# Performance work log

Measured on AMD Instinct MI355X. Metric: run time of the kernel, lower is better.

The kernel has to match this reference:

```python
import jax, jax.numpy as jnp
import numpy as np

GRID_SIZE = 5
SPLINE_ORDER = 3
N_COEFF = GRID_SIZE + SPLINE_ORDER  # 8 basis functions per input feature
D_MODEL = 1024
D_FF = 4096


def make_grid(in_features):
    # uniform grid on [-1, 1] extended by spline_order knots each side
    h = 2.0 / GRID_SIZE
    g = np.arange(-SPLINE_ORDER, GRID_SIZE + SPLINE_ORDER + 1, dtype=np.float32) * h - 1.0
    return jnp.asarray(np.tile(g[None, :], (in_features, 1)))  # (in, G + 2k + 1)


def b_splines(x, grid):
    # x: (N, in) -> (N, in, G + k) via Cox-de Boor recursion
    xe = x[..., None]
    bases = ((xe >= grid[:, :-1]) & (xe < grid[:, 1:])).astype(x.dtype)
    for j in range(1, SPLINE_ORDER + 1):
        left = (xe - grid[:, : -(j + 1)]) / (grid[:, j:-1] - grid[:, : -(j + 1)])
        right = (grid[:, j + 1 :] - xe) / (grid[:, j + 1 :] - grid[:, 1:-j])
        bases = left * bases[..., :-1] + right * bases[..., 1:]
    return bases


def kan_linear(x, base_w, spline_w, grid):
    # x: (N, in); base_w: (out, in); spline_w: (out, in, C)
    base = jax.nn.silu(x) @ base_w.T
    b = b_splines(x, grid)                      # (N, in, C)
    spl = jnp.einsum('nic,oic->no', b, spline_w)
    return base + spl


def setup_inputs() -> dict:
    key = jax.random.key(0)
    ks = jax.random.split(key, 7)
    s_in = 1.0 / np.sqrt(D_MODEL)
    s_ff = 1.0 / np.sqrt(D_FF)
    return {
        'x': jax.random.normal(ks[0], (2, 2048, D_MODEL), jnp.float32),
        'base_w1': jax.random.normal(ks[1], (D_FF, D_MODEL), jnp.float32) * s_in,
        'spline_w1': jax.random.normal(ks[2], (D_FF, D_MODEL, N_COEFF), jnp.float32) * s_in * 0.1,
        'base_w2': jax.random.normal(ks[3], (D_FF, D_MODEL), jnp.float32) * s_in,
        'spline_w2': jax.random.normal(ks[4], (D_FF, D_MODEL, N_COEFF), jnp.float32) * s_in * 0.1,
        'base_w3': jax.random.normal(ks[5], (D_MODEL, D_FF), jnp.float32) * s_ff,
        'spline_w3': jax.random.normal(ks[6], (D_MODEL, D_FF, N_COEFF), jnp.float32) * s_ff * 0.1,
        'grid_in': make_grid(D_MODEL),
        'grid_ff': make_grid(D_FF),
    }


def reference(x, base_w1, spline_w1, base_w2, spline_w2, base_w3, spline_w3, grid_in, grid_ff):
    shp = x.shape
    x2 = x.reshape(-1, shp[-1])                      # (N, d_model)
    h = kan_linear(x2, base_w1, spline_w1, grid_in) * kan_linear(x2, base_w2, spline_w2, grid_in)
    out = kan_linear(h, base_w3, spline_w3, grid_ff)
    return out.reshape(shp)
```

## Files before the change

### kernel.cpp

```cpp
#include <hip/hip_runtime.h>
#include <hip/hip_bf16.h>
#include <cstdint>
#include <cstddef>
#include <type_traits>


#define D_MODEL 1024
#define D_FF    4096
#define NTOK    4096
#define NC      9
#define K1      (D_MODEL * NC)
#define K3      (D_FF * NC)
#define SPLITK2 16
#define SPLITKF 4
#define CHUNK   1024
#define SLOT    65536

typedef __attribute__((ext_vector_type(8))) short bf16x8;
typedef __attribute__((ext_vector_type(4))) float f32x4;

__device__ __forceinline__ unsigned short bf16b(float f) {
  __hip_bfloat16 h = __float2bfloat16(f);
  return __builtin_bit_cast(unsigned short, h);
}
__device__ __forceinline__ uint32_t pk2(float a, float b) {
  return (uint32_t)bf16b(a) | ((uint32_t)bf16b(b) << 16);
}

__device__ __forceinline__ void kan_feat_u(float x, unsigned short* dst) {
  float s = x / (1.0f + __expf(-x));
  float B[11];
#pragma unroll
  for (int j = 0; j < 11; ++j) {
    float gj = -2.2f + 0.4f * j;
    B[j] = (x >= gj && x < gj + 0.4f) ? 1.0f : 0.0f;
  }
#pragma unroll
  for (int p = 1; p <= 3; ++p) {
    float inv = 1.0f / (0.4f * p);
#pragma unroll
    for (int i = 0; i + p < 11; ++i) {
      float gi = -2.2f + 0.4f * i;
      B[i] = (x - gi) * inv * B[i] + ((gi + 0.4f + 0.4f * p) - x) * inv * B[i + 1];
    }
  }
  dst[0] = bf16b(s);
#pragma unroll
  for (int c = 0; c < 8; ++c) dst[1 + c] = bf16b(B[c]);
}

__global__ void pack_kan_w(const float* __restrict__ bw, const float* __restrict__ sw,
                           __hip_bfloat16* __restrict__ W, int K, int inShift,
                           int rowMul, int rowBase, size_t totalPairs) {
  size_t t = (size_t)blockIdx.x * blockDim.x + threadIdx.x;
  if (t >= totalPairs) return;
  const int halfShift = inShift - 1;
  size_t o = t >> halfShift;
  size_t p = t & (((size_t)1 << halfShift) - 1);
  size_t e0 = (o << inShift) + 2 * p;
  float2 b = *(const float2*)(bw + e0);
  const float4* sp = (const float4*)(sw + e0 * 8);
  float4 s0 = sp[0], s1 = sp[1], s2 = sp[2], s3 = sp[3];
  const size_t HP = (size_t)1 << halfShift;
  uint32_t* dst = (uint32_t*)(W + (o * rowMul + rowBase) * (size_t)K);
  dst[p]          = pk2(b.x, b.y);
  dst[1 * HP + p] = pk2(s0.x, s2.x);
  dst[2 * HP + p] = pk2(s0.y, s2.y);
  dst[3 * HP + p] = pk2(s0.z, s2.z);
  dst[4 * HP + p] = pk2(s0.w, s2.w);
  dst[5 * HP + p] = pk2(s1.x, s3.x);
  dst[6 * HP + p] = pk2(s1.y, s3.y);
  dst[7 * HP + p] = pk2(s1.z, s3.z);
  dst[8 * HP + p] = pk2(s1.w, s3.w);
}

__global__ void build_a1(const float* __restrict__ x, __hip_bfloat16* __restrict__ A1) {
  size_t t = (size_t)blockIdx.x * blockDim.x + threadIdx.x;
  if (t >= (size_t)NTOK * D_MODEL / 2) return;
  size_t n = t >> 9;
  size_t p = t & 511;
  float2 xv = *(const float2*)(x + n * D_MODEL + 2 * p);
  unsigned short h0[9], h1[9];
  kan_feat_u(xv.x, h0);
  kan_feat_u(xv.y, h1);
  uint32_t* dst = (uint32_t*)(A1 + n * (size_t)K1);
#pragma unroll
  for (int f = 0; f < 9; ++f)
    dst[(size_t)f * 512 + p] = (uint32_t)h0[f] | ((uint32_t)h1[f] << 16);
}

template <typename HT>
__global__ void glu_a3(const HT* __restrict__ Hc, __hip_bfloat16* __restrict__ A3c) {
  size_t t = (size_t)blockIdx.x * blockDim.x + threadIdx.x;
  if (t >= (size_t)CHUNK * D_FF / 2) return;
  size_t n = t >> 11;
  size_t p = t & 2047;
  float a0, a1, c0, c1;
  if constexpr (std::is_same<HT, float>::value) {
    float2 u = *(const float2*)(Hc + n * 8192 + 2 * p);
    float2 v = *(const float2*)(Hc + n * 8192 + 4096 + 2 * p);
    a0 = u.x; a1 = u.y; c0 = v.x; c1 = v.y;
  } else {
    a0 = __bfloat162float(Hc[n * 8192 + 2 * p]);
    a1 = __bfloat162float(Hc[n * 8192 + 2 * p + 1]);
    c0 = __bfloat162float(Hc[n * 8192 + 4096 + 2 * p]);
    c1 = __bfloat162float(Hc[n * 8192 + 4096 + 2 * p + 1]);
  }
  unsigned short h0[9], h1[9];
  kan_feat_u(a0 * c0, h0);
  kan_feat_u(a1 * c1, h1);
  uint32_t* dst = (uint32_t*)(A3c + n * (size_t)K3);
#pragma unroll
  for (int f = 0; f < 9; ++f)
    dst[(size_t)f * 2048 + p] = (uint32_t)h0[f] | ((uint32_t)h1[f] << 16);
}

#define STAGE(Ts)                                                                        \
  {                                                                                      \
    const int _sl = ((Ts) & 1) * SLOT;                                                   \
    const size_t _ko = (size_t)(Ts) * 128;                                               \
    _Pragma("unroll") for (int _st = 0; _st < 4; ++_st) {                                \
      __builtin_amdgcn_global_load_lds(                                                  \
          (const __attribute__((address_space(1))) void*)(gA0 + _st * strideK + _ko),    \
          (__attribute__((address_space(3))) void*)(lds_raw + _sl + _st * 8192 + dW),    \
          16, 0, 0);                                                                     \
      __builtin_amdgcn_global_load_lds(                                                  \
          (const __attribute__((address_space(1))) void*)(gB0 + _st * strideK + _ko),    \
          (__attribute__((address_space(3))) void*)(lds_raw + _sl + 32768 +              \
                                                    _st * 8192 + dW),                    \
          16, 0, 0);                                                                     \
    }                                                                                    \
  }

template <typename CT, bool FUSE>
__global__ __launch_bounds__(512, 2) void gemm256(
    const __hip_bfloat16* __restrict__ A, const __hip_bfloat16* __restrict__ Bw,
    CT* __restrict__ Cp, int N, int K, int kLen,
    __hip_bfloat16* __restrict__ A3out) {
  __shared__ __align__(16) char lds_raw[2 * SLOT];

  const int tid = threadIdx.x;
  const int wid = tid >> 6, lane = tid & 63;
  const int wr = wid >> 2, wc = wid & 3;

  const int nwg = gridDim.x * gridDim.y;
  const int orig = blockIdx.y * gridDim.x + blockIdx.x;
  const int q = nwg >> 3, r = nwg & 7;
  const int xcd = orig & 7, lid = orig >> 3;
  const int wg = (xcd < r ? xcd * (q + 1) : r * (q + 1) + (xcd - r) * q) + lid;
  const int bx = wg % gridDim.x, by = wg / gridDim.x;

  const size_t brow = (size_t)by * 256;
  const size_t bcol = (size_t)bx * 256;
  const int kStart = (int)blockIdx.z * kLen;
  const int NT = kLen / 64;

  const int kbx = (lane & 7) ^ (lane >> 3);
  const int rsub = lane >> 3;
  const size_t strideK = (size_t)K * 128;
  const char* gA0 = (const char*)A +
      ((brow + (size_t)(wid * 8 + rsub)) * (size_t)K + kStart + kbx * 8) * 2;
  const char* gB0 = (const char*)Bw +
      ((bcol + (size_t)(wid * 8 + rsub)) * (size_t)K + kStart + kbx * 8) * 2;
  const int dW = wid * 1024;

  const int gx0 = (((lane >> 4) ^ (lane & 7))) * 16;
  const int gx1 = ((((lane >> 4) + 4) ^ (lane & 7))) * 16;
  const int arow = (wr * 128 + (lane & 15)) * 128;
  const int brw = 32768 + (wc * 64 + (lane & 15)) * 128;

  f32x4 acc[8][4] = {};

  STAGE(0);
  asm volatile("s_waitcnt vmcnt(0)" ::: "memory");
  __builtin_amdgcn_s_barrier();

  for (int T = 0; T < NT; ++T) {
    if (T + 1 < NT) STAGE(T + 1);

    const int sl = (T & 1) * SLOT;
    bf16x8 af[8], bfr[4];
#pragma unroll
    for (int mf = 0; mf < 8; ++mf)
      af[mf] = *(const bf16x8*)(lds_raw + sl + arow + mf * 2048 + gx0);
#pragma unroll
    for (int nf = 0; nf < 4; ++nf)
      bfr[nf] = *(const bf16x8*)(lds_raw + sl + brw + nf * 2048 + gx0);
    __builtin_amdgcn_s_setprio(1);
#pragma unroll
    for (int mf = 0; mf < 8; ++mf)
#pragma unroll
      for (int nf = 0; nf < 4; ++nf)
        acc[mf][nf] =
            __builtin_amdgcn_mfma_f32_16x16x32_bf16(af[mf], bfr[nf], acc[mf][nf], 0, 0, 0);
    __builtin_amdgcn_s_setprio(0);
#pragma unroll
    for (int mf = 0; mf < 8; ++mf)
      af[mf] = *(const bf16x8*)(lds_raw + sl + arow + mf * 2048 + gx1);
#pragma unroll
    for (int nf = 0; nf < 4; ++nf)
      bfr[nf] = *(const bf16x8*)(lds_raw + sl + brw + nf * 2048 + gx1);
    __builtin_amdgcn_s_setprio(1);
#pragma unroll
    for (int mf = 0; mf < 8; ++mf)
#pragma unroll
      for (int nf = 0; nf < 4; ++nf)
        acc[mf][nf] =
            __builtin_amdgcn_mfma_f32_16x16x32_bf16(af[mf], bfr[nf], acc[mf][nf], 0, 0, 0);
    __builtin_amdgcn_s_setprio(0);

    asm volatile("s_waitcnt vmcnt(0)" ::: "memory");
    asm volatile("s_waitcnt lgkmcnt(0)" ::: "memory");
    __builtin_amdgcn_s_barrier();
  }

  if constexpr (FUSE) {
    float* gbuf = (float*)lds_raw;
#pragma unroll
    for (int mf = 0; mf < 8; ++mf) {
      const int s = wr * 8 + mf;
#pragma unroll
      for (int nf = 0; nf < 4; ++nf) {
#pragma unroll
        for (int rr = 0; rr < 4; ++rr) {
          float v = acc[mf][nf][rr];
          float w = __shfl_xor(v, 1, 64);
          if (!(lane & 1)) {
            const int r4 = (lane >> 4) * 4 + rr;
            const int ploc = wc * 32 + nf * 8 + ((lane & 14) >> 1);
            gbuf[s * 2048 + r4 * 128 + ploc] = v * w;
          }
        }
      }
    }
    __builtin_amdgcn_s_barrier();
    const int p2 = tid & 63;
    const int rb = tid >> 6;
    for (int k = 0; k < 32; ++k) {
      const int rr_ = rb + 8 * k;
      const int s = rr_ >> 4, rl = rr_ & 15;
      float g0 = gbuf[s * 2048 + rl * 128 + 2 * p2];
      float g1 = gbuf[s * 2048 + rl * 128 + 2 * p2 + 1];
      unsigned short h0[9], h1[9];
      kan_feat_u(g0, h0);
      kan_feat_u(g1, h1);
      uint32_t* dst = (uint32_t*)(A3out + (brow + rr_) * (size_t)K3);
      const size_t pbase = (bcol >> 2) + p2;
#pragma unroll
      for (int f = 0; f < 9; ++f)
        dst[(size_t)f * 2048 + pbase] = (uint32_t)h0[f] | ((uint32_t)h1[f] << 16);
    }
  } else {
#pragma unroll
    for (int mf = 0; mf < 8; ++mf)
#pragma unroll
      for (int nf = 0; nf < 4; ++nf) {
        const size_t r0 = brow + wr * 128 + mf * 16 + (lane >> 4) * 4;
        const size_t c0 = bcol + wc * 64 + nf * 16 + (lane & 15);
        const size_t M = (size_t)gridDim.y * 256;
        CT* C = Cp + (size_t)blockIdx.z * M * (size_t)N;
#pragma unroll
        for (int rr = 0; rr < 4; ++rr) {
          float v = acc[mf][nf][rr];
          if constexpr (std::is_same<CT, float>::value)
            C[(r0 + rr) * (size_t)N + c0] = v;
          else
            C[(r0 + rr) * (size_t)N + c0] = __float2bfloat16(v);
        }
      }
  }
}

__global__ void reduceK(const float* __restrict__ P, float* __restrict__ out,
                        size_t quarter, int nslice) {
  size_t t = (size_t)blockIdx.x * blockDim.x + threadIdx.x;
  if (t >= quarter) return;
  const float4* p = (const float4*)P;
  float4 a = p[t];
  for (int s = 1; s < nslice; ++s) {
    float4 b = p[(size_t)s * quarter + t];
    a.x += b.x; a.y += b.y; a.z += b.z; a.w += b.w;
  }
  ((float4*)out)[t] = a;
}

extern "C" void kernel_launch(void* const* d_in, const int* in_sizes, int n_in,
                              void* d_out, int out_size, void* d_ws, size_t ws_size,
                              hipStream_t stream) {
  const float* x   = (const float*)d_in[0];
  const float* bw1 = (const float*)d_in[1];
  const float* sw1 = (const float*)d_in[2];
  const float* bw2 = (const float*)d_in[3];
  const float* sw2 = (const float*)d_in[4];
  const float* bw3 = (const float*)d_in[5];
  const float* sw3 = (const float*)d_in[6];
  float* out = (float*)d_out;
  char* ws = (char*)d_ws;

  const size_t W12_B  = (size_t)8192 * K1 * 2;
  const size_t A1_B   = (size_t)NTOK * K1 * 2;
  const size_t A3F_B  = (size_t)NTOK * K3 * 2;
  const size_t A3C_B  = (size_t)CHUNK * K3 * 2;
  const size_t HF32_B = (size_t)NTOK * 8192 * 4;

  const bool fused = ws_size >= W12_B + A1_B + A3F_B;
  const bool hF32  = ws_size >= W12_B + A1_B + HF32_B;

  __hip_bfloat16* W12 = (__hip_bfloat16*)(ws);
  __hip_bfloat16* A1  = (__hip_bfloat16*)(ws + W12_B);
  __hip_bfloat16* W3  = A1;

  size_t pairs12 = (size_t)D_FF * D_MODEL / 2;
  int blocks12 = (int)((pairs12 + 255) / 256);
  size_t pairs3 = (size_t)D_MODEL * D_FF / 2;
  int blocks3 = (int)((pairs3 + 255) / 256);
  size_t pairsA1 = (size_t)NTOK * D_MODEL / 2;

  if (fused) {
    __hip_bfloat16* A3f = (__hip_bfloat16*)(ws + W12_B + A1_B);
    float*          Par = (float*)(ws);

    pack_kan_w<<<blocks12, 256, 0, stream>>>(bw1, sw1, W12, K1, 10, 2, 0, pairs12);
    pack_kan_w<<<blocks12, 256, 0, stream>>>(bw2, sw2, W12, K1, 10, 2, 1, pairs12);
    build_a1<<<(int)((pairsA1 + 255) / 256), 256, 0, stream>>>(x, A1);
    gemm256<float, true><<<dim3(8192 / 256, NTOK / 256, 1), 512, 0, stream>>>(
        A1, W12, nullptr, 8192, K1, K1, A3f);
    pack_kan_w<<<blocks3, 256, 0, stream>>>(bw3, sw3, W3, K3, 12, 1, 0, pairs3);
    gemm256<float, false><<<dim3(D_MODEL / 256, NTOK / 256, SPLITKF), 512, 0, stream>>>(
        A3f, W3, Par, D_MODEL, K3, K3 / SPLITKF, nullptr);
    size_t quarter = (size_t)NTOK * D_MODEL / 4;
    reduceK<<<(int)((quarter + 255) / 256), 256, 0, stream>>>(Par, out, quarter, SPLITKF);
  } else {
    void*           Hv  = (void*)(ws + W12_B + A1_B);
    __hip_bfloat16* A3c = (__hip_bfloat16*)(ws);
    float*          Par = (float*)(ws + A3C_B);

    pack_kan_w<<<blocks12, 256, 0, stream>>>(bw1, sw1, W12, K1, 10, 1, 0, pairs12);
    pack_kan_w<<<blocks12, 256, 0, stream>>>(bw2, sw2, W12, K1, 10, 1, 4096, pairs12);
    build_a1<<<(int)((pairsA1 + 255) / 256), 256, 0, stream>>>(x, A1);
    if (hF32)
      gemm256<float, false><<<dim3(8192 / 256, NTOK / 256, 1), 512, 0, stream>>>(
          A1, W12, (float*)Hv, 8192, K1, K1, nullptr);
    else
      gemm256<__hip_bfloat16, false><<<dim3(8192 / 256, NTOK / 256, 1), 512, 0, stream>>>(
          A1, W12, (__hip_bfloat16*)Hv, 8192, K1, K1, nullptr);
    pack_kan_w<<<blocks3, 256, 0, stream>>>(bw3, sw3, W3, K3, 12, 1, 0, pairs3);
    for (int c = 0; c < NTOK / CHUNK; ++c) {
      size_t pairsG = (size_t)CHUNK * D_FF / 2;
      int blocksG = (int)((pairsG + 255) / 256);
      if (hF32)
        glu_a3<float><<<blocksG, 256, 0, stream>>>(
            (const float*)Hv + (size_t)c * CHUNK * 8192, A3c);
      else
        glu_a3<__hip_bfloat16><<<blocksG, 256, 0, stream>>>(
            (const __hip_bfloat16*)Hv + (size_t)c * CHUNK * 8192, A3c);
      gemm256<float, false><<<dim3(D_MODEL / 256, CHUNK / 256, SPLITK2), 512, 0, stream>>>(
          A3c, W3, Par, D_MODEL, K3, K3 / SPLITK2, nullptr);
      size_t quarter = (size_t)CHUNK * D_MODEL / 4;
      reduceK<<<(int)((quarter + 255) / 256), 256, 0, stream>>>(
          Par, out + (size_t)c * CHUNK * D_MODEL, quarter, SPLITK2);
    }
  }
}
```

Measured before the change: 1.012 ms.

## Restructure GEMM main loop into 8-phase pipeline with interleaved half-tile staging

Result: faster. 966.2 us (-4.6%).

```diff
diff --git a/kernel.cpp b/kernel.cpp
--- a/kernel.cpp
+++ b/kernel.cpp
@@ -14,10 +14,12 @@
 #define SPLITK2 16
 #define SPLITKF 4
 #define CHUNK   1024
-#define SLOT    65536
 
 typedef __attribute__((ext_vector_type(8))) short bf16x8;
 typedef __attribute__((ext_vector_type(4))) float f32x4;
+
+#define AS1 __attribute__((address_space(1)))
+#define AS3 __attribute__((address_space(3)))
 
 __device__ __forceinline__ unsigned short bf16b(float f) {
   __hip_bfloat16 h = __float2bfloat16(f);
@@ -115,29 +117,79 @@
     dst[(size_t)f * 2048 + p] = (uint32_t)h0[f] | ((uint32_t)h1[f] << 16);
 }
 
-#define STAGE(Ts)                                                                        \
+#define LDSA(D, MF, GX) \
+  (*(const bf16x8*)(lds_raw + (D)*65536 + aoffH + (MF)*2048 + (GX)))
+#define LDSB(D, NF, GX) \
+  (*(const bf16x8*)(lds_raw + (D)*65536 + boffH + (NF)*2048 + (GX)))
+
+#define STAGE_A(KK, H)                                                                   \
   {                                                                                      \
-    const int _sl = ((Ts) & 1) * SLOT;                                                   \
-    const size_t _ko = (size_t)(Ts) * 128;                                               \
-    _Pragma("unroll") for (int _st = 0; _st < 4; ++_st) {                                \
-      __builtin_amdgcn_global_load_lds(                                                  \
-          (const __attribute__((address_space(1))) void*)(gA0 + _st * strideK + _ko),    \
-          (__attribute__((address_space(3))) void*)(lds_raw + _sl + _st * 8192 + dW),    \
-          16, 0, 0);                                                                     \
-      __builtin_amdgcn_global_load_lds(                                                  \
-          (const __attribute__((address_space(1))) void*)(gB0 + _st * strideK + _ko),    \
-          (__attribute__((address_space(3))) void*)(lds_raw + _sl + 32768 +              \
-                                                    _st * 8192 + dW),                    \
-          16, 0, 0);                                                                     \
+    const size_t _s = (size_t)(H) * 128 * strideRow + (size_t)(KK) * 128;                \
+    const int _d = (((KK) & 1) * 65536) + ((H) * 32768) + dT;                            \
+    __builtin_amdgcn_global_load_lds((const AS1 void*)(gAb + _s),                        \
+                                     (AS3 void*)(lds_raw + _d), 16, 0, 0);               \
+    __builtin_amdgcn_global_load_lds((const AS1 void*)(gAb + _s + 64 * strideRow),       \
+                                     (AS3 void*)(lds_raw + _d + 8192), 16, 0, 0);        \
+  }
+#define STAGE_B(KK, H)                                                                   \
+  {                                                                                      \
+    const size_t _s = (size_t)(H) * 128 * strideRow + (size_t)(KK) * 128;                \
+    const int _d = (((KK) & 1) * 65536) + ((H) * 32768) + 16384 + dT;                    \
+    __builtin_amdgcn_global_load_lds((const AS1 void*)(gBb + _s),                        \
+                                     (AS3 void*)(lds_raw + _d), 16, 0, 0);               \
+    __builtin_amdgcn_global_load_lds((const AS1 void*)(gBb + _s + 64 * strideRow),       \
+                                     (AS3 void*)(lds_raw + _d + 8192), 16, 0, 0);        \
+  }
+
+#define MF16(P)                                                                          \
+  __builtin_amdgcn_s_setprio(1);                                                         \
+  _Pragma("unroll") for (int _m = 0; _m < 2; ++_m)                                       \
+      _Pragma("unroll") for (int _n = 0; _n < 4; ++_n) {                                 \
+    acc[2 * (P) + _m][_n] = __builtin_amdgcn_mfma_f32_16x16x32_bf16(                     \
+        af[_m][0], bfr[_n][0], acc[2 * (P) + _m][_n], 0, 0, 0);                          \
+    acc[2 * (P) + _m][_n] = __builtin_amdgcn_mfma_f32_16x16x32_bf16(                     \
+        af[_m][1], bfr[_n][1], acc[2 * (P) + _m][_n], 0, 0, 0);                          \
+  }                                                                                      \
+  __builtin_amdgcn_s_setprio(0);
+
+#define PH0(D, STG, WT)                                                                  \
+  {                                                                                      \
+    _Pragma("unroll") for (int _n = 0; _n < 4; ++_n) {                                   \
+      bfr[_n][0] = LDSB(D, _n, gx0);                                                     \
+      bfr[_n][1] = LDSB(D, _n, gx1);                                                     \
     }                                                                                    \
-  }
+    af[0][0] = LDSA(D, 0, gx0); af[0][1] = LDSA(D, 0, gx1);                              \
+    af[1][0] = LDSA(D, 1, gx0); af[1][1] = LDSA(D, 1, gx1);                              \
+    STG;                                                                                 \
+    __builtin_amdgcn_s_barrier();                                                        \
+    asm volatile("s_waitcnt lgkmcnt(0)" ::: "memory");                                   \
+    __builtin_amdgcn_sched_barrier(0);                                                   \
+    MF16(0);                                                                             \
+    WT;                                                                                  \
+    __builtin_amdgcn_s_barrier();                                                        \
+  }
+#define PHN(D, P, STG, WT)                                                               \
+  {                                                                                      \
+    af[0][0] = LDSA(D, 2 * (P), gx0);     af[0][1] = LDSA(D, 2 * (P), gx1);              \
+    af[1][0] = LDSA(D, 2 * (P) + 1, gx0); af[1][1] = LDSA(D, 2 * (P) + 1, gx1);          \
+    STG;                                                                                 \
+    __builtin_amdgcn_s_barrier();                                                        \
+    asm volatile("s_waitcnt lgkmcnt(0)" ::: "memory");                                   \
+    __builtin_amdgcn_sched_barrier(0);                                                   \
+    MF16(P);                                                                             \
+    WT;                                                                                  \
+    __builtin_amdgcn_s_barrier();                                                        \
+  }
+
+#define VM4 asm volatile("s_waitcnt vmcnt(4)" ::: "memory")
+#define VM0 asm volatile("s_waitcnt vmcnt(0)" ::: "memory")
 
 template <typename CT, bool FUSE>
 __global__ __launch_bounds__(512, 2) void gemm256(
     const __hip_bfloat16* __restrict__ A, const __hip_bfloat16* __restrict__ Bw,
     CT* __restrict__ Cp, int N, int K, int kLen,
     __hip_bfloat16* __restrict__ A3out) {
-  __shared__ __align__(16) char lds_raw[2 * SLOT];
+  __shared__ __align__(16) char lds_raw[131072];
 
   const int tid = threadIdx.x;
   const int wid = tid >> 6, lane = tid & 63;
@@ -155,63 +207,37 @@
   const int kStart = (int)blockIdx.z * kLen;
   const int NT = kLen / 64;
 
-  const int kbx = (lane & 7) ^ (lane >> 3);
-  const int rsub = lane >> 3;
-  const size_t strideK = (size_t)K * 128;
-  const char* gA0 = (const char*)A +
-      ((brow + (size_t)(wid * 8 + rsub)) * (size_t)K + kStart + kbx * 8) * 2;
-  const char* gB0 = (const char*)Bw +
-      ((bcol + (size_t)(wid * 8 + rsub)) * (size_t)K + kStart + kbx * 8) * 2;
-  const int dW = wid * 1024;
+  const int kbx = (tid & 7) ^ ((tid >> 3) & 7);
+  const size_t strideRow = (size_t)K * 2;
+  const char* gAb = (const char*)A + ((brow + (size_t)(tid >> 3)) * (size_t)K + kStart) * 2 + kbx * 16;
+  const char* gBb = (const char*)Bw + ((bcol + (size_t)(tid >> 3)) * (size_t)K + kStart) * 2 + kbx * 16;
+  const int dT = tid * 16;
 
   const int gx0 = (((lane >> 4) ^ (lane & 7))) * 16;
   const int gx1 = ((((lane >> 4) + 4) ^ (lane & 7))) * 16;
-  const int arow = (wr * 128 + (lane & 15)) * 128;
-  const int brw = 32768 + (wc * 64 + (lane & 15)) * 128;
+  const int aoffH = wr * 32768 + (lane & 15) * 128;
+  const int boffH = (wc >> 1) * 32768 + 16384 + ((wc & 1) * 64 + (lane & 15)) * 128;
 
   f32x4 acc[8][4] = {};
-
-  STAGE(0);
-  asm volatile("s_waitcnt vmcnt(0)" ::: "memory");
+  bf16x8 af[2][2], bfr[4][2];
+
+  STAGE_B(0, 0); STAGE_B(0, 1);
+  STAGE_A(0, 0); STAGE_A(0, 1);
+  STAGE_B(1, 0); STAGE_B(1, 1);
+  VM4;
   __builtin_amdgcn_s_barrier();
 
-  for (int T = 0; T < NT; ++T) {
-    if (T + 1 < NT) STAGE(T + 1);
-
-    const int sl = (T & 1) * SLOT;
-    bf16x8 af[8], bfr[4];
-#pragma unroll
-    for (int mf = 0; mf < 8; ++mf)
-      af[mf] = *(const bf16x8*)(lds_raw + sl + arow + mf * 2048 + gx0);
-#pragma unroll
-    for (int nf = 0; nf < 4; ++nf)
-      bfr[nf] = *(const bf16x8*)(lds_raw + sl + brw + nf * 2048 + gx0);
-    __builtin_amdgcn_s_setprio(1);
-#pragma unroll
-    for (int mf = 0; mf < 8; ++mf)
-#pragma unroll
-      for (int nf = 0; nf < 4; ++nf)
-        acc[mf][nf] =
-            __builtin_amdgcn_mfma_f32_16x16x32_bf16(af[mf], bfr[nf], acc[mf][nf], 0, 0, 0);
-    __builtin_amdgcn_s_setprio(0);
-#pragma unroll
-    for (int mf = 0; mf < 8; ++mf)
-      af[mf] = *(const bf16x8*)(lds_raw + sl + arow + mf * 2048 + gx1);
-#pragma unroll
-    for (int nf = 0; nf < 4; ++nf)
-      bfr[nf] = *(const bf16x8*)(lds_raw + sl + brw + nf * 2048 + gx1);
-    __builtin_amdgcn_s_setprio(1);
-#pragma unroll
-    for (int mf = 0; mf < 8; ++mf)
-#pragma unroll
-      for (int nf = 0; nf < 4; ++nf)
-        acc[mf][nf] =
-            __builtin_amdgcn_mfma_f32_16x16x32_bf16(af[mf], bfr[nf], acc[mf][nf], 0, 0, 0);
-    __builtin_amdgcn_s_setprio(0);
-
-    asm volatile("s_waitcnt vmcnt(0)" ::: "memory");
-    asm volatile("s_waitcnt lgkmcnt(0)" ::: "memory");
-    __builtin_amdgcn_s_barrier();
+  for (int i = 0; i < NT / 2; ++i) {
+    const int a = 2 * i;
+    const bool nl = (i != NT / 2 - 1);
+    PH0(0, STAGE_A(a + 1, 0), );
+    PHN(0, 1, STAGE_A(a + 1, 1), );
+    PHN(0, 2, if (nl) STAGE_B(a + 2, 0), );
+    PHN(0, 3, if (nl) STAGE_B(a + 2, 1), if (nl) { VM4; } else { VM0; });
+    PH0(1, if (nl) STAGE_A(a + 2, 0), );
+    PHN(1, 1, if (nl) STAGE_A(a + 2, 1), );
+    PHN(1, 2, if (nl) STAGE_B(a + 3, 0), );
+    PHN(1, 3, if (nl) STAGE_B(a + 3, 1), if (nl) { VM4; } else { VM0; });
   }
 
   if constexpr (FUSE) {
```
